# Kernel tuning notes

Hardware: AMD Instinct MI355X
Metric: run time of the kernel (lower is better)

Reference implementation:

```python
import jax, jax.numpy as jnp
import numpy as np

STACK = 1000            # stackSize (number of stacked TT networks, e.g. relations)
L = (8, 8, 8)           # input_fac[0]: left mode sizes  -> nRow = 512
R = (8, 8, 8)           # input_fac[1]: right mode sizes -> nCol = 512
RANKS = (16, 16)        # internal TT ranks (boundary ranks of 1 are dropped)
B = 512                 # batch of indices


def setup_inputs() -> dict:
    key = jax.random.key(0)
    k0, k1, k2, ki = jax.random.split(key, 4)
    # torch.rand(coreSize) * 0.1  ->  uniform[0, 0.1)
    core0 = jax.random.uniform(k0, (STACK, L[0], R[0], RANKS[0]), dtype=jnp.float32) * 0.1
    core1 = jax.random.uniform(k1, (STACK, RANKS[0], L[1], R[1], RANKS[1]), dtype=jnp.float32) * 0.1
    core2 = jax.random.uniform(k2, (STACK, RANKS[1], L[2], R[2]), dtype=jnp.float32) * 0.1
    indices = jax.random.randint(ki, (B,), 0, STACK, dtype=jnp.int64 if jax.config.read('jax_enable_x64') else jnp.int32)
    return {"core0": core0, "core1": core1, "core2": core2, "indices": indices}


def reference(core0, core1, core2, indices):
    # Gather the per-index TT cores
    c0 = core0[indices]  # [b, l0, r0, k1]
    c1 = core1[indices]  # [b, k1, l1, r1, k2]
    c2 = core2[indices]  # [b, k2, l2, r2]
    # Sequential TT-chain contraction over rank axes k1 then k2.
    # ncon out_order = [batch, l0, l1, l2, r0, r1, r2]
    t = jnp.einsum('baik,bkcjm->bacijm', c0, c1)        # [b, l0, l1, r0, r1, k2]
    out = jnp.einsum('bacijm,bmdl->bacdijl', t, c2)     # [b, l0, l1, l2, r0, r1, r2]
    nRow = L[0] * L[1] * L[2]
    nCol = R[0] * R[1] * R[2]
    return out.reshape(indices.shape[0], nRow, nCol)
```

## Files before the change

kernel.cpp:

```cpp
#include <hip/hip_runtime.h>
#include <stdint.h>


typedef short short8 __attribute__((ext_vector_type(8)));
typedef float f32x4 __attribute__((ext_vector_type(4)));

__device__ __forceinline__ float bflo(uint32_t u) { return __uint_as_float(u << 16); }
__device__ __forceinline__ float bfhi(uint32_t u) { return __uint_as_float(u & 0xffff0000u); }
__device__ __forceinline__ uint32_t pack_bf2(float f0, float f1) {
  uint32_t a = __float_as_uint(f0) + 0x8000u;
  uint32_t b = __float_as_uint(f1) + 0x8000u;
  return (a >> 16) | (b & 0xffff0000u);
}

__global__ __launch_bounds__(256) void tt_stack_kernel(
    const float* __restrict__ c0f,
    const float* __restrict__ c1f,
    const float* __restrict__ c2f,
    const int* __restrict__ idx,
    float* __restrict__ outf)
{
  __shared__ __align__(16) uint32_t lds_c1[8192];
  __shared__ __align__(16) float    lds_c0[128];
  __shared__ __align__(16) uint32_t lds_c2b[1024];
  __shared__ __align__(16) uint32_t lds_t[4096];

  const int tid = threadIdx.x;
  const int bid = blockIdx.x;
  const int b = bid >> 3;
  const int a = bid & 7;
  const int s = idx[b];
  const size_t s1024 = (size_t)s * 1024;

  {
    const float4* src4 = (const float4*)(c1f + (size_t)s * 16384);
#pragma unroll
    for (int r = 0; r < 16; ++r) {
      const float4 v = src4[r * 256 + tid];
      uint2* dst = (uint2*)&lds_c1[2 * (r * 256 + tid)];
      *dst = make_uint2(pack_bf2(v.x, v.y), pack_bf2(v.z, v.w));
    }
  }
  if (tid < 128) lds_c0[tid] = c0f[(size_t)(s * 8 + a) * 128 + tid];
#pragma unroll
  for (int rep = 0; rep < 2; ++rep) {
    const int t2 = tid + rep * 256;
    const int w = t2 & 7;
    const int col = t2 >> 3;
    const float v0 = c2f[s1024 + (size_t)(2 * w) * 64 + col];
    const float v1 = c2f[s1024 + (size_t)(2 * w + 1) * 64 + col];
    const uint32_t h0 = (__float_as_uint(v0) + 0x8000u) & 0xffff0000u;
    const uint32_t h1 = (__float_as_uint(v1) + 0x8000u) & 0xffff0000u;
    lds_c2b[col * 16 + w] = (h0 >> 16) | h1;
    lds_c2b[col * 16 + 8 + w] =
        pack_bf2(v0 - __uint_as_float(h0), v1 - __uint_as_float(h1));
  }
  __syncthreads();

  const int sw = (tid >> 2) & 1;
#pragma unroll
  for (int cc = 0; cc < 2; ++cc) {
    const int combo = tid + cc * 256;
    const int c = combo >> 6;
    const int i = (combo >> 3) & 7;
    const int j = combo & 7;
    float a_k[16];
#pragma unroll
    for (int k = 0; k < 16; ++k) a_k[k] = lds_c0[i * 16 + k];
    float acc[16];
#pragma unroll
    for (int m = 0; m < 16; ++m) acc[m] = 0.f;
#pragma unroll
    for (int k = 0; k < 16; ++k) {
      const uint4* rp = (const uint4*)&lds_c1[((k * 8 + c) * 8 + j) * 8];
      const uint4 u0 = rp[0];
      const uint4 u1 = rp[1];
      const float av = a_k[k];
      acc[0]  = fmaf(av, bflo(u0.x), acc[0]);   acc[1]  = fmaf(av, bfhi(u0.x), acc[1]);
      acc[2]  = fmaf(av, bflo(u0.y), acc[2]);   acc[3]  = fmaf(av, bfhi(u0.y), acc[3]);
      acc[4]  = fmaf(av, bflo(u0.z), acc[4]);   acc[5]  = fmaf(av, bfhi(u0.z), acc[5]);
      acc[6]  = fmaf(av, bflo(u0.w), acc[6]);   acc[7]  = fmaf(av, bfhi(u0.w), acc[7]);
      acc[8]  = fmaf(av, bflo(u1.x), acc[8]);   acc[9]  = fmaf(av, bfhi(u1.x), acc[9]);
      acc[10] = fmaf(av, bflo(u1.y), acc[10]);  acc[11] = fmaf(av, bfhi(u1.y), acc[11]);
      acc[12] = fmaf(av, bflo(u1.z), acc[12]);  acc[13] = fmaf(av, bfhi(u1.z), acc[13]);
      acc[14] = fmaf(av, bflo(u1.w), acc[14]);  acc[15] = fmaf(av, bfhi(u1.w), acc[15]);
    }
    uint32_t* tb = &lds_t[combo * 8];
    *(uint4*)&tb[sw * 4] =
        make_uint4(pack_bf2(acc[0], acc[1]),  pack_bf2(acc[2], acc[3]),
                   pack_bf2(acc[4], acc[5]),  pack_bf2(acc[6], acc[7]));
    *(uint4*)&tb[4 - sw * 4] =
        make_uint4(pack_bf2(acc[8], acc[9]),  pack_bf2(acc[10], acc[11]),
                   pack_bf2(acc[12], acc[13]), pack_bf2(acc[14], acc[15]));
  }
  __syncthreads();

  const int lane = tid & 63, wv = tid >> 6;
  const int g = lane >> 4, lcol = lane & 15;
  short8 Afr[4];
#pragma unroll
  for (int rt = 0; rt < 4; ++rt)
    Afr[rt] = *(const short8*)&lds_c2b[(rt * 16 + lcol) * 16 + g * 4];
  const int hsel = (g & 1) ^ ((lcol >> 2) & 1);
  float* const outa = outf + (size_t)b * 262144 + a * 32768;

#pragma unroll
  for (int ctl = 0; ctl < 8; ++ctl) {
    const int cix = wv * 128 + ctl * 16 + lcol;
    const short8 bv8 = *(const short8*)&lds_t[cix * 8 + hsel * 4];
    const int cq = cix >> 6;
    const int klo = cix & 63;
    float* const op0 = outa + (size_t)(cq * 8 + (g >> 1)) * 512
                            + klo * 8 + (g & 1) * 4;
#pragma unroll
    for (int rt = 0; rt < 4; ++rt) {
      f32x4 dd = {0.f, 0.f, 0.f, 0.f};
      dd = __builtin_amdgcn_mfma_f32_16x16x32_bf16(Afr[rt], bv8, dd, 0, 0, 0);
      __builtin_nontemporal_store(dd, (f32x4*)(op0 + rt * 1024));
    }
  }
}

extern "C" void kernel_launch(void* const* d_in, const int* in_sizes, int n_in,
                              void* d_out, int out_size, void* d_ws, size_t ws_size,
                              hipStream_t stream) {
  const float* c0f = (const float*)d_in[0];
  const float* c1f = (const float*)d_in[1];
  const float* c2f = (const float*)d_in[2];
  const int* idx = (const int*)d_in[3];
  float* outf = (float*)d_out;
  const int B = in_sizes[3];
  dim3 grid(B * 8), block(256);
  hipLaunchKernelGGL(tt_stack_kernel, grid, block, 0, stream, c0f, c1f, c2f, idx, outf);
}
```

Before: 581.0 us.

## Drop LDS staging of cores, read c1/c0/c2 directly from global per wave

The kernel no longer stages core1, core0 and core2 through shared memory. Each wave loads its own slice of c1 in fp32 straight from global memory, keeps c0 in registers, and builds the MFMA A fragments for c2 directly in registers. Two block barriers go away and LDS use shrinks to the 16 KB t buffer. Launch bounds now request 4 blocks per CU, and the block index mapping is swapped so consecutive blocks share the same a slice across different batch items. The cost is more global/L2 traffic for c1 (fp32, duplicated reads across the 8 blocks per index) and the removal of the full c1 unroll.

```diff
diff --git a/kernel.cpp b/kernel.cpp
--- a/kernel.cpp
+++ b/kernel.cpp
@@ -5,87 +5,93 @@
 typedef short short8 __attribute__((ext_vector_type(8)));
 typedef float f32x4 __attribute__((ext_vector_type(4)));
 
-__device__ __forceinline__ float bflo(uint32_t u) { return __uint_as_float(u << 16); }
-__device__ __forceinline__ float bfhi(uint32_t u) { return __uint_as_float(u & 0xffff0000u); }
 __device__ __forceinline__ uint32_t pack_bf2(float f0, float f1) {
   uint32_t a = __float_as_uint(f0) + 0x8000u;
   uint32_t b = __float_as_uint(f1) + 0x8000u;
   return (a >> 16) | (b & 0xffff0000u);
 }
 
-__global__ __launch_bounds__(256) void tt_stack_kernel(
+__global__ __launch_bounds__(256, 4) void tt_stack_kernel(
     const float* __restrict__ c0f,
     const float* __restrict__ c1f,
     const float* __restrict__ c2f,
     const int* __restrict__ idx,
     float* __restrict__ outf)
 {
-  __shared__ __align__(16) uint32_t lds_c1[8192];
-  __shared__ __align__(16) float    lds_c0[128];
-  __shared__ __align__(16) uint32_t lds_c2b[1024];
   __shared__ __align__(16) uint32_t lds_t[4096];
 
   const int tid = threadIdx.x;
   const int bid = blockIdx.x;
-  const int b = bid >> 3;
-  const int a = bid & 7;
+  const int b = bid & 511;
+  const int a = bid >> 9;
   const int s = idx[b];
   const size_t s1024 = (size_t)s * 1024;
 
+  const int lane = tid & 63, wv = tid >> 6;
+  const int g = lane >> 4, lcol = lane & 15;
+
+  short8 Afr[4];
   {
-    const float4* src4 = (const float4*)(c1f + (size_t)s * 16384);
+    const float* c2s = c2f + s1024 + (size_t)((g & 1) * 8) * 64;
 #pragma unroll
-    for (int r = 0; r < 16; ++r) {
-      const float4 v = src4[r * 256 + tid];
-      uint2* dst = (uint2*)&lds_c1[2 * (r * 256 + tid)];
-      *dst = make_uint2(pack_bf2(v.x, v.y), pack_bf2(v.z, v.w));
+    for (int rt = 0; rt < 4; ++rt) {
+      const int col = rt * 16 + lcol;
+      uint32_t w[4];
+#pragma unroll
+      for (int p = 0; p < 4; ++p) {
+        const float v0 = c2s[(2 * p) * 64 + col];
+        const float v1 = c2s[(2 * p + 1) * 64 + col];
+        const uint32_t h0 = (__float_as_uint(v0) + 0x8000u) & 0xffff0000u;
+        const uint32_t h1 = (__float_as_uint(v1) + 0x8000u) & 0xffff0000u;
+        const uint32_t hip = (h0 >> 16) | h1;
+        const uint32_t lop = pack_bf2(v0 - __uint_as_float(h0),
+                                      v1 - __uint_as_float(h1));
+        w[p] = (g < 2) ? hip : lop;
+      }
+      uint4 wq = make_uint4(w[0], w[1], w[2], w[3]);
+      Afr[rt] = *reinterpret_cast<short8*>(&wq);
     }
   }
-  if (tid < 128) lds_c0[tid] = c0f[(size_t)(s * 8 + a) * 128 + tid];
+
+  const int i = (lane >> 3) & 7, j = lane & 7;
+  float c0v[16];
+  {
+    const float* c0s = c0f + (size_t)(s * 8 + a) * 128 + i * 16;
 #pragma unroll
-  for (int rep = 0; rep < 2; ++rep) {
-    const int t2 = tid + rep * 256;
-    const int w = t2 & 7;
-    const int col = t2 >> 3;
-    const float v0 = c2f[s1024 + (size_t)(2 * w) * 64 + col];
-    const float v1 = c2f[s1024 + (size_t)(2 * w + 1) * 64 + col];
-    const uint32_t h0 = (__float_as_uint(v0) + 0x8000u) & 0xffff0000u;
-    const uint32_t h1 = (__float_as_uint(v1) + 0x8000u) & 0xffff0000u;
-    lds_c2b[col * 16 + w] = (h0 >> 16) | h1;
-    lds_c2b[col * 16 + 8 + w] =
-        pack_bf2(v0 - __uint_as_float(h0), v1 - __uint_as_float(h1));
+    for (int q = 0; q < 4; ++q)
+      *(f32x4*)&c0v[q * 4] = *(const f32x4*)(c0s + q * 4);
   }
-  __syncthreads();
 
-  const int sw = (tid >> 2) & 1;
+  const int sw = (lane >> 2) & 1;
+  const int hsel = (g & 1) ^ ((lcol >> 2) & 1);
+  float* const outa = outf + (size_t)b * 262144 + a * 32768;
+
 #pragma unroll
   for (int cc = 0; cc < 2; ++cc) {
-    const int combo = tid + cc * 256;
-    const int c = combo >> 6;
-    const int i = (combo >> 3) & 7;
-    const int j = combo & 7;
-    float a_k[16];
-#pragma unroll
-    for (int k = 0; k < 16; ++k) a_k[k] = lds_c0[i * 16 + k];
+    const int row = wv * 128 + cc * 64 + lane;
+    const int c = wv * 2 + cc;
+    const float* c1r = c1f + (size_t)s * 16384 + (size_t)(c * 8 + j) * 16;
     float acc[16];
 #pragma unroll
     for (int m = 0; m < 16; ++m) acc[m] = 0.f;
-#pragma unroll
+#pragma unroll 2
     for (int k = 0; k < 16; ++k) {
-      const uint4* rp = (const uint4*)&lds_c1[((k * 8 + c) * 8 + j) * 8];
-      const uint4 u0 = rp[0];
-      const uint4 u1 = rp[1];
-      const float av = a_k[k];
-      acc[0]  = fmaf(av, bflo(u0.x), acc[0]);   acc[1]  = fmaf(av, bfhi(u0.x), acc[1]);
-      acc[2]  = fmaf(av, bflo(u0.y), acc[2]);   acc[3]  = fmaf(av, bfhi(u0.y), acc[3]);
-      acc[4]  = fmaf(av, bflo(u0.z), acc[4]);   acc[5]  = fmaf(av, bfhi(u0.z), acc[5]);
-      acc[6]  = fmaf(av, bflo(u0.w), acc[6]);   acc[7]  = fmaf(av, bfhi(u0.w), acc[7]);
-      acc[8]  = fmaf(av, bflo(u1.x), acc[8]);   acc[9]  = fmaf(av, bfhi(u1.x), acc[9]);
-      acc[10] = fmaf(av, bflo(u1.y), acc[10]);  acc[11] = fmaf(av, bfhi(u1.y), acc[11]);
-      acc[12] = fmaf(av, bflo(u1.z), acc[12]);  acc[13] = fmaf(av, bfhi(u1.z), acc[13]);
-      acc[14] = fmaf(av, bflo(u1.w), acc[14]);  acc[15] = fmaf(av, bfhi(u1.w), acc[15]);
+      const f32x4* rp = (const f32x4*)(c1r + (size_t)k * 1024);
+      const f32x4 v0 = rp[0];
+      const f32x4 v1 = rp[1];
+      const f32x4 v2 = rp[2];
+      const f32x4 v3 = rp[3];
+      const float av = c0v[k];
+      acc[0]  = fmaf(av, v0[0], acc[0]);   acc[1]  = fmaf(av, v0[1], acc[1]);
+      acc[2]  = fmaf(av, v0[2], acc[2]);   acc[3]  = fmaf(av, v0[3], acc[3]);
+      acc[4]  = fmaf(av, v1[0], acc[4]);   acc[5]  = fmaf(av, v1[1], acc[5]);
+      acc[6]  = fmaf(av, v1[2], acc[6]);   acc[7]  = fmaf(av, v1[3], acc[7]);
+      acc[8]  = fmaf(av, v2[0], acc[8]);   acc[9]  = fmaf(av, v2[1], acc[9]);
+      acc[10] = fmaf(av, v2[2], acc[10]);  acc[11] = fmaf(av, v2[3], acc[11]);
+      acc[12] = fmaf(av, v3[0], acc[12]);  acc[13] = fmaf(av, v3[1], acc[13]);
+      acc[14] = fmaf(av, v3[2], acc[14]);  acc[15] = fmaf(av, v3[3], acc[15]);
     }
-    uint32_t* tb = &lds_t[combo * 8];
+    uint32_t* tb = &lds_t[row * 8];
     *(uint4*)&tb[sw * 4] =
         make_uint4(pack_bf2(acc[0], acc[1]),  pack_bf2(acc[2], acc[3]),
                    pack_bf2(acc[4], acc[5]),  pack_bf2(acc[6], acc[7]));
@@ -93,16 +99,6 @@
         make_uint4(pack_bf2(acc[8], acc[9]),  pack_bf2(acc[10], acc[11]),
                    pack_bf2(acc[12], acc[13]), pack_bf2(acc[14], acc[15]));
   }
-  __syncthreads();
-
-  const int lane = tid & 63, wv = tid >> 6;
-  const int g = lane >> 4, lcol = lane & 15;
-  short8 Afr[4];
-#pragma unroll
-  for (int rt = 0; rt < 4; ++rt)
-    Afr[rt] = *(const short8*)&lds_c2b[(rt * 16 + lcol) * 16 + g * 4];
-  const int hsel = (g & 1) ^ ((lcol >> 2) & 1);
-  float* const outa = outf + (size_t)b * 262144 + a * 32768;
 
 #pragma unroll
   for (int ctl = 0; ctl < 8; ++ctl) {
```

Result: slower. 615.5 us (+5.9%).
